# Kernel optimization log

Hardware: AMD Instinct MI355X
Metric: run time of the kernel (lower is better)

## Reference

```python
import jax, jax.numpy as jnp
import numpy as np

N, NFEAT, NHID, NCLASS, NHEAD = 8192, 512, 64, 16, 4
ALPHA = 0.1  # leaky relu slope
NEG = -9e15


def setup_inputs() -> dict:
    key = jax.random.key(0)
    ks = jax.random.split(key, 7)
    x = jax.random.normal(ks[0], (N, NFEAT), dtype=jnp.float32)
    adj = (jax.random.uniform(ks[1], (N, N)) < 0.05).astype(jnp.float32)
    # per-head params: W [H, nfeat, nhid], a [H, 2*nhid] (xavier-ish scale)
    W = jax.random.normal(ks[2], (NHEAD, NFEAT, NHID), dtype=jnp.float32) * (1.0 / np.sqrt(NFEAT))
    a = jax.random.normal(ks[3], (NHEAD, 2 * NHID), dtype=jnp.float32) * (1.0 / np.sqrt(NHID))
    W_out = jax.random.normal(ks[4], (NHEAD * NHID, NCLASS), dtype=jnp.float32) * (1.0 / np.sqrt(NHEAD * NHID))
    a_out = jax.random.normal(ks[5], (2 * NCLASS,), dtype=jnp.float32) * (1.0 / np.sqrt(NCLASS))
    return {"x": x, "adj": adj, "W": W, "a": a, "W_out": W_out, "a_out": a_out}


def _gat_layer(h, adj, Wk, ak):
    """Dense pyGAT GraphAttentionLayer (eval mode, dropout = identity)."""
    d = Wk.shape[1]
    Wh = h @ Wk                         # [N, d]
    f1 = Wh @ ak[:d]                    # [N]
    f2 = Wh @ ak[d:]                    # [N]
    e = jax.nn.leaky_relu(f1[:, None] + f2[None, :], negative_slope=ALPHA)  # [N, N]
    att = jax.nn.softmax(jnp.where(adj > 0, e, NEG), axis=1)
    return att @ Wh                     # [N, d]


def reference(x, adj, W, a, W_out, a_out):
    # eval mode: F.dropout is identity
    heads = jax.vmap(lambda Wk, ak: jax.nn.elu(_gat_layer(x, adj, Wk, ak)))(W, a)  # [H, N, nhid]
    h = jnp.transpose(heads, (1, 0, 2)).reshape(x.shape[0], -1)                    # [N, H*nhid]
    out = jax.nn.elu(_gat_layer(h, adj, W_out, a_out))                             # [N, nclass]
    return jax.nn.log_softmax(out, axis=1)
```

## Files before the change

kernel.cpp:

```cpp
#include <hip/hip_runtime.h>
#include <hip/hip_bf16.h>

#define NN 8192
#define NFEAT 512
#define NHID 64
#define NCLASS 16
#define NHEAD 4
#define ALPHA 0.1f
#define CAP 768

typedef short bf16x8 __attribute__((ext_vector_type(8)));
typedef float f32x4 __attribute__((ext_vector_type(4)));

__device__ __forceinline__ float lrelu(float x) { return fmaxf(x, ALPHA * x); }
__device__ __forceinline__ float elu(float x) { return x > 0.f ? x : __expf(x) - 1.f; }
__device__ __forceinline__ short f2b(float x) {
  union { __bf16 b; short s; } c; c.b = (__bf16)x; return c.s;
}
__device__ __forceinline__ float b2f(short x) {
  union { unsigned int u; float f; } c; c.u = ((unsigned int)(unsigned short)x) << 16; return c.f;
}

#define UPF(w, v, A0, A1)                                  \
  {                                                        \
    const float lo_ = __uint_as_float((v) << 16);          \
    const float hi_ = __uint_as_float((v) & 0xffff0000u);  \
    (A0) += (w) * lo_;                                     \
    (A1) += (w) * hi_;                                     \
  }

__global__ __launch_bounds__(256) void k_wprep(const float* __restrict__ W,
                                               short* __restrict__ WB) {
  __shared__ float t[64][65];
  const int h = blockIdx.y;
  const int k0 = blockIdx.x * 64;
  const int tid = threadIdx.x;
#pragma unroll
  for (int it = 0; it < 16; ++it) {
    const int r = it * 4 + (tid >> 6), c = tid & 63;
    t[r][c] = W[((size_t)h * NFEAT + k0 + r) * NHID + c];
  }
  __syncthreads();
#pragma unroll
  for (int it = 0; it < 16; ++it) {
    const int d = it * 4 + (tid >> 6), k = tid & 63;
    WB[((size_t)h * NHID + d) * NFEAT + k0 + k] = f2b(t[k][d]);
  }
}

__global__ __launch_bounds__(256) void k_mega1(const float* __restrict__ adj,
                                               unsigned int* __restrict__ bmask,
                                               const float* __restrict__ x,
                                               const short* __restrict__ WB,
                                               const float* __restrict__ a,
                                               short* __restrict__ WhB,
                                               float* __restrict__ f1,
                                               float* __restrict__ f2i) {
  const int tid = threadIdx.x;
  if (blockIdx.x < 2048) {
    const float4* a4 = reinterpret_cast<const float4*>(adj);
    const int t0 = blockIdx.x * 256 + tid;
#pragma unroll 4
    for (int it = 0; it < 32; ++it) {
      const int g = it * 524288 + t0;
      const float4 v = a4[g];
      unsigned int nv = (unsigned int)((v.x > 0.f) | ((v.y > 0.f) << 1) |
                                       ((v.z > 0.f) << 2) | ((v.w > 0.f) << 3))
                        << ((tid & 7) * 4);
      nv |= __shfl_xor(nv, 1);
      nv |= __shfl_xor(nv, 2);
      nv |= __shfl_xor(nv, 4);
      if ((tid & 7) == 0) bmask[g >> 3] = nv;
    }
    return;
  }
  __shared__ short tile[64][72];
  const int bid = blockIdx.x - 2048;
  const int h = bid >> 7;
  const int bm = (bid & 127) * 64;
  const int wv = tid >> 6, lane = tid & 63;
  const int mr = lane & 15, kg = lane >> 4;
  f32x4 acc0 = {0.f, 0.f, 0.f, 0.f}, acc1 = acc0, acc2 = acc0, acc3 = acc0;
  const float* ap = x + (size_t)(bm + wv * 16 + mr) * NFEAT + kg * 8;
  const short* bp = WB + ((size_t)h * NHID + mr) * NFEAT + kg * 8;
#pragma unroll 2
  for (int k0 = 0; k0 < NFEAT; k0 += 32) {
    const float4 xa = *reinterpret_cast<const float4*>(ap);
    const float4 xb = *reinterpret_cast<const float4*>(ap + 4);
    bf16x8 af;
    af[0] = f2b(xa.x); af[1] = f2b(xa.y); af[2] = f2b(xa.z); af[3] = f2b(xa.w);
    af[4] = f2b(xb.x); af[5] = f2b(xb.y); af[6] = f2b(xb.z); af[7] = f2b(xb.w);
    const bf16x8 b0 = *reinterpret_cast<const bf16x8*>(bp);
    const bf16x8 b1 = *reinterpret_cast<const bf16x8*>(bp + 16 * NFEAT);
    const bf16x8 b2 = *reinterpret_cast<const bf16x8*>(bp + 32 * NFEAT);
    const bf16x8 b3 = *reinterpret_cast<const bf16x8*>(bp + 48 * NFEAT);
    acc0 = __builtin_amdgcn_mfma_f32_16x16x32_bf16(af, b0, acc0, 0, 0, 0);
    acc1 = __builtin_amdgcn_mfma_f32_16x16x32_bf16(af, b1, acc1, 0, 0, 0);
    acc2 = __builtin_amdgcn_mfma_f32_16x16x32_bf16(af, b2, acc2, 0, 0, 0);
    acc3 = __builtin_amdgcn_mfma_f32_16x16x32_bf16(af, b3, acc3, 0, 0, 0);
    ap += 32; bp += 32;
  }
  float a1v[4], a2v[4];
#pragma unroll
  for (int c = 0; c < 4; ++c) {
    a1v[c] = a[h * 128 + mr + c * 16];
    a2v[c] = a[h * 128 + 64 + mr + c * 16];
  }
#pragma unroll
  for (int q = 0; q < 4; ++q) {
    float s1 = acc0[q] * a1v[0] + acc1[q] * a1v[1] + acc2[q] * a1v[2] + acc3[q] * a1v[3];
    float s2 = acc0[q] * a2v[0] + acc1[q] * a2v[1] + acc2[q] * a2v[2] + acc3[q] * a2v[3];
#pragma unroll
    for (int off = 1; off < 16; off <<= 1) {
      s1 += __shfl_xor(s1, off);
      s2 += __shfl_xor(s2, off);
    }
    if (mr == 0) {
      const int i = bm + wv * 16 + kg * 4 + q;
      f1[h * NN + i] = s1;
      f2i[(size_t)i * 4 + h] = s2;
    }
  }
#pragma unroll
  for (int q = 0; q < 4; ++q) {
    const int r = wv * 16 + kg * 4 + q;
    tile[r][mr +  0] = f2b(acc0[q]);
    tile[r][mr + 16] = f2b(acc1[q]);
    tile[r][mr + 32] = f2b(acc2[q]);
    tile[r][mr + 48] = f2b(acc3[q]);
  }
  __syncthreads();
  {
    const int row = tid >> 2, seg = tid & 3;
    bf16x8 o0, o1;
#pragma unroll
    for (int u = 0; u < 8; ++u) {
      o0[u] = tile[row][seg * 16 + u];
      o1[u] = tile[row][seg * 16 + 8 + u];
    }
    short* dst = WhB + (size_t)(bm + row) * 256 + h * 64 + seg * 16;
    *reinterpret_cast<bf16x8*>(dst) = o0;
    *reinterpret_cast<bf16x8*>(dst + 8) = o1;
  }
}

__global__ __launch_bounds__(256) void k_rmax(const float* __restrict__ src,
                                              float* __restrict__ dst, int n, int stride,
                                              int boff) {
  const float* p = src + (size_t)blockIdx.x * boff;
  float m = -1e30f;
  for (int k = threadIdx.x; k < n; k += 256) m = fmaxf(m, p[(size_t)k * stride]);
#pragma unroll
  for (int off = 32; off; off >>= 1) m = fmaxf(m, __shfl_xor(m, off));
  __shared__ float sm[4];
  if ((threadIdx.x & 63) == 0) sm[threadIdx.x >> 6] = m;
  __syncthreads();
  if (threadIdx.x == 0) dst[blockIdx.x] = fmaxf(fmaxf(sm[0], sm[1]), fmaxf(sm[2], sm[3]));
}

__global__ __launch_bounds__(256) void k_attn1b(const unsigned int* __restrict__ bmask,
                                                const short* __restrict__ WhB,
                                                const float* __restrict__ f1,
                                                const float* __restrict__ f2i,
                                                const float* __restrict__ f2max,
                                                short* __restrict__ hcat) {
  __shared__ unsigned short idx[CAP];
  __shared__ unsigned int widx[NHEAD][CAP];
  __shared__ float swp[4][NHEAD];
  __shared__ float sinv[NHEAD];
  __shared__ int cnt;
  const int i = blockIdx.x;
  const int tid = threadIdx.x;
  const int wv = tid >> 6, lane = tid & 63;
  if (tid == 0) cnt = 0;
  __syncthreads();

  {
    unsigned int word = bmask[(size_t)i * 256 + tid];
    const int c = __popc(word);
    if (c) {
      int base = atomicAdd(&cnt, c);
      const int j0 = tid * 32;
      while (word) {
        const int b = __ffs(word) - 1;
        word &= word - 1;
        if (base < CAP) idx[base++] = (unsigned short)(j0 + b);
      }
    }
  }
  __syncthreads();
  const int n = min(cnt, CAP);

  float f1r[NHEAD], mrow[NHEAD], sw[NHEAD] = {0.f, 0.f, 0.f, 0.f};
#pragma unroll
  for (int h = 0; h < NHEAD; ++h) {
    f1r[h] = f1[h * NN + i];
    mrow[h] = lrelu(f1r[h] + f2max[h]);
  }
  for (int k = tid; k < n; k += 256) {
    const int j = idx[k];
    const float4 f = *reinterpret_cast<const float4*>(f2i + (size_t)j * 4);
    const float w0 = __expf(lrelu(f1r[0] + f.x) - mrow[0]);
    const float w1 = __expf(lrelu(f1r[1] + f.y) - mrow[1]);
    const float w2 = __expf(lrelu(f1r[2] + f.z) - mrow[2]);
    const float w3 = __expf(lrelu(f1r[3] + f.w) - mrow[3]);
    widx[0][k] = ((unsigned int)(unsigned short)f2b(w0) << 16) | (unsigned int)j;
    widx[1][k] = ((unsigned int)(unsigned short)f2b(w1) << 16) | (unsigned int)j;
    widx[2][k] = ((unsigned int)(unsigned short)f2b(w2) << 16) | (unsigned int)j;
    widx[3][k] = ((unsigned int)(unsigned short)f2b(w3) << 16) | (unsigned int)j;
    sw[0] += w0; sw[1] += w1; sw[2] += w2; sw[3] += w3;
  }
#pragma unroll
  for (int off = 32; off; off >>= 1)
#pragma unroll
    for (int h = 0; h < NHEAD; ++h) sw[h] += __shfl_xor(sw[h], off);
  if (lane == 0) {
#pragma unroll
    for (int h = 0; h < NHEAD; ++h) swp[wv][h] = sw[h];
  }
  __syncthreads();
  if (tid < NHEAD) sinv[tid] = 1.f / (swp[0][tid] + swp[1][tid] + swp[2][tid] + swp[3][tid]);

  const int g = lane >> 3, l = lane & 7;
  float acc[8] = {};
  const short* wb = WhB + wv * 64 + l * 8;
  const unsigned int* wrow = widx[wv];
#pragma unroll 2
  for (int k = g; k < n; k += 16) {
    const unsigned int v0 = wrow[k];
    const int k1 = k + 8;
    const unsigned int v1 = (k1 < n) ? wrow[k1] : 0u;
    const int j0 = v0 & 0xffffu;
    const float w0 = __uint_as_float(v0 & 0xffff0000u);
    const int j1 = v1 & 0xffffu;
    const float w1 = __uint_as_float(v1 & 0xffff0000u);
    const uint4 e0 = *reinterpret_cast<const uint4*>(wb + (size_t)j0 * 256);
    const uint4 e1 = *reinterpret_cast<const uint4*>(wb + (size_t)j1 * 256);
    UPF(w0, e0.x, acc[0], acc[1])
    UPF(w0, e0.y, acc[2], acc[3])
    UPF(w0, e0.z, acc[4], acc[5])
    UPF(w0, e0.w, acc[6], acc[7])
    UPF(w1, e1.x, acc[0], acc[1])
    UPF(w1, e1.y, acc[2], acc[3])
    UPF(w1, e1.z, acc[4], acc[5])
    UPF(w1, e1.w, acc[6], acc[7])
  }
  __syncthreads();
#pragma unroll
  for (int u = 0; u < 8; ++u) {
    acc[u] += __shfl_xor(acc[u], 8);
    acc[u] += __shfl_xor(acc[u], 16);
    acc[u] += __shfl_xor(acc[u], 32);
  }
  if (lane < 8) {
    const float iv = sinv[wv];
    bf16x8 o;
#pragma unroll
    for (int u = 0; u < 8; ++u) o[u] = f2b(elu(acc[u] * iv));
    *reinterpret_cast<bf16x8*>(hcat + (size_t)i * 256 + wv * 64 + lane * 8) = o;
  }
}

__global__ __launch_bounds__(256) void k_gemm2(const short* __restrict__ hcat,
                                               const float* __restrict__ Wout,
                                               const float* __restrict__ aout,
                                               short* __restrict__ Wh2B,
                                               float* __restrict__ f1o,
                                               float* __restrict__ f2o) {
  __shared__ float sW[NHEAD * NHID][NCLASS + 1];
  __shared__ float sh[16][NHEAD * NHID + 1];
  const int tid = threadIdx.x;
  const int r = tid >> 4, c = tid & 15;
  const int row = blockIdx.x * 16 + r;
  for (int u = tid; u < 256 * 16; u += 256) sW[u >> 4][u & 15] = Wout[u];
  for (int u = tid; u < 16 * 256; u += 256)
    sh[u >> 8][u & 255] = b2f(hcat[(size_t)(blockIdx.x * 16 + (u >> 8)) * 256 + (u & 255)]);
  __syncthreads();
  float acc = 0.f;
#pragma unroll 8
  for (int f = 0; f < 256; ++f) acc += sh[r][f] * sW[f][c];
  Wh2B[(size_t)row * NCLASS + c] = f2b(acc);
  float s1 = acc * aout[c];
  float s2 = acc * aout[NCLASS + c];
#pragma unroll
  for (int off = 8; off; off >>= 1) { s1 += __shfl_xor(s1, off); s2 += __shfl_xor(s2, off); }
  if (c == 0) { f1o[row] = s1; f2o[row] = s2; }
}

__global__ __launch_bounds__(256) void k_attn2(const unsigned int* __restrict__ bmask,
                                               const short* __restrict__ Wh2B,
                                               const float* __restrict__ f1o,
                                               const float* __restrict__ f2o,
                                               const float* __restrict__ f2omax,
                                               float* __restrict__ out) {
  __shared__ unsigned short idx[CAP];
  __shared__ unsigned int wj[CAP];
  __shared__ float red[4][NCLASS];
  __shared__ float swp[4];
  __shared__ float sinvs;
  __shared__ int cnt;
  const int i = blockIdx.x;
  const int tid = threadIdx.x;
  const int wv = tid >> 6, lane = tid & 63;
  if (tid == 0) cnt = 0;
  __syncthreads();

  {
    unsigned int word = bmask[(size_t)i * 256 + tid];
    const int c = __popc(word);
    if (c) {
      int base = atomicAdd(&cnt, c);
      const int j0 = tid * 32;
      while (word) {
        const int b = __ffs(word) - 1;
        word &= word - 1;
        if (base < CAP) idx[base++] = (unsigned short)(j0 + b);
      }
    }
  }
  __syncthreads();
  const int n = min(cnt, CAP);

  const float f1r = f1o[i];
  const float mrow = lrelu(f1r + f2omax[0]);
  float sw = 0.f;
  for (int k = tid; k < n; k += 256) {
    const int j = idx[k];
    const float w = __expf(lrelu(f1r + f2o[j]) - mrow);
    wj[k] = ((unsigned int)(unsigned short)f2b(w) << 16) | (unsigned int)j;
    sw += w;
  }
#pragma unroll
  for (int off = 32; off; off >>= 1) sw += __shfl_xor(sw, off);
  if (lane == 0) swp[wv] = sw;
  __syncthreads();
  if (tid == 0) sinvs = 1.f / (swp[0] + swp[1] + swp[2] + swp[3]);

  const int g = tid >> 2, gl = tid & 3;
  float acc[4] = {};
  for (int k = g; k < n; k += 128) {
    const unsigned int v0 = wj[k];
    const int k1 = k + 64;
    const unsigned int v1 = (k1 < n) ? wj[k1] : 0u;
    const int j0 = v0 & 0xffffu;
    const float w0 = __uint_as_float(v0 & 0xffff0000u);
    const int j1 = v1 & 0xffffu;
    const float w1 = __uint_as_float(v1 & 0xffff0000u);
    const uint2 e0 = *reinterpret_cast<const uint2*>(Wh2B + (size_t)j0 * NCLASS + gl * 4);
    const uint2 e1 = *reinterpret_cast<const uint2*>(Wh2B + (size_t)j1 * NCLASS + gl * 4);
    UPF(w0, e0.x, acc[0], acc[1])
    UPF(w0, e0.y, acc[2], acc[3])
    UPF(w1, e1.x, acc[0], acc[1])
    UPF(w1, e1.y, acc[2], acc[3])
  }
  __syncthreads();
#pragma unroll
  for (int u = 0; u < 4; ++u) {
    acc[u] += __shfl_xor(acc[u], 4);
    acc[u] += __shfl_xor(acc[u], 8);
    acc[u] += __shfl_xor(acc[u], 16);
    acc[u] += __shfl_xor(acc[u], 32);
  }
  if (lane < 4) {
#pragma unroll
    for (int u = 0; u < 4; ++u) red[wv][lane * 4 + u] = acc[u];
  }
  __syncthreads();
  if (tid < NCLASS) {
    const float s = red[0][tid] + red[1][tid] + red[2][tid] + red[3][tid];
    const float v = elu(s * sinvs);
    float vm = v;
#pragma unroll
    for (int off = 8; off; off >>= 1) vm = fmaxf(vm, __shfl_xor(vm, off, 16));
    float ex = __expf(v - vm);
#pragma unroll
    for (int off = 8; off; off >>= 1) ex += __shfl_xor(ex, off, 16);
    out[(size_t)i * NCLASS + tid] = v - vm - __logf(ex);
  }
}

extern "C" void kernel_launch(void* const* d_in, const int* in_sizes, int n_in,
                              void* d_out, int out_size, void* d_ws, size_t ws_size,
                              hipStream_t stream) {
  const float* x    = (const float*)d_in[0];
  const float* adj  = (const float*)d_in[1];
  const float* W    = (const float*)d_in[2];
  const float* a    = (const float*)d_in[3];
  const float* Wout = (const float*)d_in[4];
  const float* aout = (const float*)d_in[5];
  float* out = (float*)d_out;
  char* ws = (char*)d_ws;
  const size_t MB = 1048576;

  unsigned int* bmask  = (unsigned int*)(ws);
  short* WhB           = (short*)(ws + 8 * MB);
  short* hcat          = (short*)(ws + 12 * MB);
  short* WB            = (short*)(ws + 16 * MB);
  float* f1            = (float*)(ws + 16 * MB + 262144);
  float* f2i           = (float*)(ws + 16 * MB + 393216);
  float* f1o           = (float*)(ws + 16 * MB + 524288);
  float* f2o           = (float*)(ws + 16 * MB + 557056);
  short* Wh2B          = (short*)(ws + 16 * MB + 589824);
  float* f2max         = (float*)(ws + 16 * MB + 851968);
  float* f2omax        = (float*)(ws + 16 * MB + 852032);

  k_wprep<<<dim3(8, 4), 256, 0, stream>>>(W, WB);
  k_mega1<<<2048 + 512, 256, 0, stream>>>(adj, bmask, x, WB, a, WhB, f1, f2i);
  k_rmax<<<NHEAD, 256, 0, stream>>>(f2i, f2max, NN, 4, 1);
  k_attn1b<<<NN, 256, 0, stream>>>(bmask, WhB, f1, f2i, f2max, hcat);
  k_gemm2<<<NN / 16, 256, 0, stream>>>(hcat, Wout, aout, Wh2B, f1o, f2o);
  k_rmax<<<1, 256, 0, stream>>>(f2o, f2omax, NN, 1, 0);
  k_attn2<<<NN, 256, 0, stream>>>(bmask, Wh2B, f1o, f2o, f2omax, out);
}
```

Before: 244.6 us.

## Fuse adjacency bitmask build into layer-1 attention, computing weights during scan

The dense adjacency scan moves out of the first prep kernel and into the per-row layer-1 attention kernel. Each block reads its own adj row with nontemporal loads, writes the bitmask for layer 2, and computes the softmax weights inline while compacting neighbours, so the separate idx pass is gone. The gather loop now reads four packed weight/index entries per uint4 and issues four row loads per iteration. f1 is stored interleaved per node, and one sync is dropped by computing the inverse sum per lane. The adj streaming now sits inside the attention kernel rather than running alongside the GEMM blocks, so it depends on that kernel keeping enough memory traffic in flight.

```diff
diff --git a/kernel.cpp b/kernel.cpp
--- a/kernel.cpp
+++ b/kernel.cpp
@@ -11,6 +11,7 @@
 
 typedef short bf16x8 __attribute__((ext_vector_type(8)));
 typedef float f32x4 __attribute__((ext_vector_type(4)));
+typedef float fv4 __attribute__((ext_vector_type(4)));
 
 __device__ __forceinline__ float lrelu(float x) { return fmaxf(x, ALPHA * x); }
 __device__ __forceinline__ float elu(float x) { return x > 0.f ? x : __expf(x) - 1.f; }
@@ -48,36 +49,17 @@
   }
 }
 
-__global__ __launch_bounds__(256) void k_mega1(const float* __restrict__ adj,
-                                               unsigned int* __restrict__ bmask,
-                                               const float* __restrict__ x,
+__global__ __launch_bounds__(256) void k_prep1(const float* __restrict__ x,
                                                const short* __restrict__ WB,
                                                const float* __restrict__ a,
                                                short* __restrict__ WhB,
-                                               float* __restrict__ f1,
+                                               float* __restrict__ f1i,
                                                float* __restrict__ f2i) {
-  const int tid = threadIdx.x;
-  if (blockIdx.x < 2048) {
-    const float4* a4 = reinterpret_cast<const float4*>(adj);
-    const int t0 = blockIdx.x * 256 + tid;
-#pragma unroll 4
-    for (int it = 0; it < 32; ++it) {
-      const int g = it * 524288 + t0;
-      const float4 v = a4[g];
-      unsigned int nv = (unsigned int)((v.x > 0.f) | ((v.y > 0.f) << 1) |
-                                       ((v.z > 0.f) << 2) | ((v.w > 0.f) << 3))
-                        << ((tid & 7) * 4);
-      nv |= __shfl_xor(nv, 1);
-      nv |= __shfl_xor(nv, 2);
-      nv |= __shfl_xor(nv, 4);
-      if ((tid & 7) == 0) bmask[g >> 3] = nv;
-    }
-    return;
-  }
   __shared__ short tile[64][72];
-  const int bid = blockIdx.x - 2048;
+  const int bid = blockIdx.x;
   const int h = bid >> 7;
   const int bm = (bid & 127) * 64;
+  const int tid = threadIdx.x;
   const int wv = tid >> 6, lane = tid & 63;
   const int mr = lane & 15, kg = lane >> 4;
   f32x4 acc0 = {0.f, 0.f, 0.f, 0.f}, acc1 = acc0, acc2 = acc0, acc3 = acc0;
@@ -117,7 +99,7 @@
     }
     if (mr == 0) {
       const int i = bm + wv * 16 + kg * 4 + q;
-      f1[h * NN + i] = s1;
+      f1i[(size_t)i * 4 + h] = s1;
       f2i[(size_t)i * 4 + h] = s2;
     }
   }
@@ -158,16 +140,15 @@
   if (threadIdx.x == 0) dst[blockIdx.x] = fmaxf(fmaxf(sm[0], sm[1]), fmaxf(sm[2], sm[3]));
 }
 
-__global__ __launch_bounds__(256) void k_attn1b(const unsigned int* __restrict__ bmask,
+__global__ __launch_bounds__(256) void k_attn1f(const float* __restrict__ adj,
                                                 const short* __restrict__ WhB,
-                                                const float* __restrict__ f1,
+                                                const float* __restrict__ f1i,
                                                 const float* __restrict__ f2i,
                                                 const float* __restrict__ f2max,
-                                                short* __restrict__ hcat) {
-  __shared__ unsigned short idx[CAP];
-  __shared__ unsigned int widx[NHEAD][CAP];
-  __shared__ float swp[4][NHEAD];
-  __shared__ float sinv[NHEAD];
+                                                short* __restrict__ hcat,
+                                                unsigned int* __restrict__ bmask) {
+  __shared__ unsigned int widx[NHEAD][CAP + 4];
+  __shared__ float swred[4][NHEAD];
   __shared__ int cnt;
   const int i = blockIdx.x;
   const int tid = threadIdx.x;
@@ -175,77 +156,91 @@
   if (tid == 0) cnt = 0;
   __syncthreads();
 
-  {
-    unsigned int word = bmask[(size_t)i * 256 + tid];
-    const int c = __popc(word);
+  const float4 f1v = *reinterpret_cast<const float4*>(f1i + (size_t)i * 4);
+  const float4 fmx = *reinterpret_cast<const float4*>(f2max);
+  float f1r[4], mrow[4], sw[4] = {0.f, 0.f, 0.f, 0.f};
+  f1r[0] = f1v.x; f1r[1] = f1v.y; f1r[2] = f1v.z; f1r[3] = f1v.w;
+  mrow[0] = lrelu(f1r[0] + fmx.x);
+  mrow[1] = lrelu(f1r[1] + fmx.y);
+  mrow[2] = lrelu(f1r[2] + fmx.z);
+  mrow[3] = lrelu(f1r[3] + fmx.w);
+
+  const fv4* arow = reinterpret_cast<const fv4*>(adj + (size_t)i * NN);
+  const float4* f2i4 = reinterpret_cast<const float4*>(f2i);
+  unsigned int* brow = bmask + (size_t)i * 256;
+#pragma unroll
+  for (int s = 0; s < 8; ++s) {
+    const fv4 v = __builtin_nontemporal_load(arow + s * 256 + tid);
+    const int b0 = v.x > 0.f, b1 = v.y > 0.f, b2 = v.z > 0.f, b3 = v.w > 0.f;
+    unsigned int nv = (unsigned int)(b0 | (b1 << 1) | (b2 << 2) | (b3 << 3)) << ((tid & 7) * 4);
+    nv |= __shfl_xor(nv, 1);
+    nv |= __shfl_xor(nv, 2);
+    nv |= __shfl_xor(nv, 4);
+    if ((tid & 7) == 0) brow[s * 32 + (tid >> 3)] = nv;
+    const int c = b0 + b1 + b2 + b3;
     if (c) {
       int base = atomicAdd(&cnt, c);
-      const int j0 = tid * 32;
-      while (word) {
-        const int b = __ffs(word) - 1;
-        word &= word - 1;
-        if (base < CAP) idx[base++] = (unsigned short)(j0 + b);
+      const int j = s * 1024 + tid * 4;
+      const int bits[4] = {b0, b1, b2, b3};
+#pragma unroll
+      for (int u = 0; u < 4; ++u) {
+        if (bits[u] && base < CAP) {
+          const int jj = j + u;
+          const float4 f = f2i4[jj];
+          const float w0 = __expf(lrelu(f1r[0] + f.x) - mrow[0]);
+          const float w1 = __expf(lrelu(f1r[1] + f.y) - mrow[1]);
+          const float w2 = __expf(lrelu(f1r[2] + f.z) - mrow[2]);
+          const float w3 = __expf(lrelu(f1r[3] + f.w) - mrow[3]);
+          widx[0][base] = ((unsigned int)(unsigned short)f2b(w0) << 16) | (unsigned int)jj;
+          widx[1][base] = ((unsigned int)(unsigned short)f2b(w1) << 16) | (unsigned int)jj;
+          widx[2][base] = ((unsigned int)(unsigned short)f2b(w2) << 16) | (unsigned int)jj;
+          widx[3][base] = ((unsigned int)(unsigned short)f2b(w3) << 16) | (unsigned int)jj;
+          sw[0] += w0; sw[1] += w1; sw[2] += w2; sw[3] += w3;
+          ++base;
+        }
       }
     }
   }
   __syncthreads();
   const int n = min(cnt, CAP);
-
-  float f1r[NHEAD], mrow[NHEAD], sw[NHEAD] = {0.f, 0.f, 0.f, 0.f};
-#pragma unroll
-  for (int h = 0; h < NHEAD; ++h) {
-    f1r[h] = f1[h * NN + i];
-    mrow[h] = lrelu(f1r[h] + f2max[h]);
-  }
-  for (int k = tid; k < n; k += 256) {
-    const int j = idx[k];
-    const float4 f = *reinterpret_cast<const float4*>(f2i + (size_t)j * 4);
-    const float w0 = __expf(lrelu(f1r[0] + f.x) - mrow[0]);
-    const float w1 = __expf(lrelu(f1r[1] + f.y) - mrow[1]);
-    const float w2 = __expf(lrelu(f1r[2] + f.z) - mrow[2]);
-    const float w3 = __expf(lrelu(f1r[3] + f.w) - mrow[3]);
-    widx[0][k] = ((unsigned int)(unsigned short)f2b(w0) << 16) | (unsigned int)j;
-    widx[1][k] = ((unsigned int)(unsigned short)f2b(w1) << 16) | (unsigned int)j;
-    widx[2][k] = ((unsigned int)(unsigned short)f2b(w2) << 16) | (unsigned int)j;
-    widx[3][k] = ((unsigned int)(unsigned short)f2b(w3) << 16) | (unsigned int)j;
-    sw[0] += w0; sw[1] += w1; sw[2] += w2; sw[3] += w3;
-  }
+  if (tid < 16) widx[tid >> 2][n + (tid & 3)] = 0;
 #pragma unroll
   for (int off = 32; off; off >>= 1)
 #pragma unroll
     for (int h = 0; h < NHEAD; ++h) sw[h] += __shfl_xor(sw[h], off);
   if (lane == 0) {
 #pragma unroll
-    for (int h = 0; h < NHEAD; ++h) swp[wv][h] = sw[h];
-  }
-  __syncthreads();
-  if (tid < NHEAD) sinv[tid] = 1.f / (swp[0][tid] + swp[1][tid] + swp[2][tid] + swp[3][tid]);
+    for (int h = 0; h < NHEAD; ++h) swred[wv][h] = sw[h];
+  }
+  __syncthreads();
 
   const int g = lane >> 3, l = lane & 7;
   float acc[8] = {};
   const short* wb = WhB + wv * 64 + l * 8;
   const unsigned int* wrow = widx[wv];
-#pragma unroll 2
-  for (int k = g; k < n; k += 16) {
-    const unsigned int v0 = wrow[k];
-    const int k1 = k + 8;
-    const unsigned int v1 = (k1 < n) ? wrow[k1] : 0u;
-    const int j0 = v0 & 0xffffu;
-    const float w0 = __uint_as_float(v0 & 0xffff0000u);
-    const int j1 = v1 & 0xffffu;
-    const float w1 = __uint_as_float(v1 & 0xffff0000u);
+  for (int k0 = g * 4; k0 < n; k0 += 32) {
+    const uint4 pw = *reinterpret_cast<const uint4*>(wrow + k0);
+    const int j0 = pw.x & 0xffffu;
+    const int j1 = pw.y & 0xffffu;
+    const int j2 = pw.z & 0xffffu;
+    const int j3 = pw.w & 0xffffu;
+    const float w0 = __uint_as_float(pw.x & 0xffff0000u);
+    const float w1 = __uint_as_float(pw.y & 0xffff0000u);
+    const float w2 = __uint_as_float(pw.z & 0xffff0000u);
+    const float w3 = __uint_as_float(pw.w & 0xffff0000u);
     const uint4 e0 = *reinterpret_cast<const uint4*>(wb + (size_t)j0 * 256);
     const uint4 e1 = *reinterpret_cast<const uint4*>(wb + (size_t)j1 * 256);
-    UPF(w0, e0.x, acc[0], acc[1])
-    UPF(w0, e0.y, acc[2], acc[3])
-    UPF(w0, e0.z, acc[4], acc[5])
-    UPF(w0, e0.w, acc[6], acc[7])
-    UPF(w1, e1.x, acc[0], acc[1])
-    UPF(w1, e1.y, acc[2], acc[3])
-    UPF(w1, e1.z, acc[4], acc[5])
-    UPF(w1, e1.w, acc[6], acc[7])
-  }
-  __syncthreads();
+    const uint4 e2 = *reinterpret_cast<const uint4*>(wb + (size_t)j2 * 256);
+    const uint4 e3 = *reinterpret_cast<const uint4*>(wb + (size_t)j3 * 256);
+    UPF(w0, e0.x, acc[0], acc[1]) UPF(w0, e0.y, acc[2], acc[3])
+    UPF(w0, e0.z, acc[4], acc[5]) UPF(w0, e0.w, acc[6], acc[7])
+    UPF(w1, e1.x, acc[0], acc[1]) UPF(w1, e1.y, acc[2], acc[3])
+    UPF(w1, e1.z, acc[4], acc[5]) UPF(w1, e1.w, acc[6], acc[7])
+    UPF(w2, e2.x, acc[0], acc[1]) UPF(w2, e2.y, acc[2], acc[3])
+    UPF(w2, e2.z, acc[4], acc[5]) UPF(w2, e2.w, acc[6], acc[7])
+    UPF(w3, e3.x, acc[0], acc[1]) UPF(w3, e3.y, acc[2], acc[3])
+    UPF(w3, e3.z, acc[4], acc[5]) UPF(w3, e3.w, acc[6], acc[7])
+  }
 #pragma unroll
   for (int u = 0; u < 8; ++u) {
     acc[u] += __shfl_xor(acc[u], 8);
@@ -253,7 +248,7 @@
     acc[u] += __shfl_xor(acc[u], 32);
   }
   if (lane < 8) {
-    const float iv = sinv[wv];
+    const float iv = 1.f / (swred[0][wv] + swred[1][wv] + swred[2][wv] + swred[3][wv]);
     bf16x8 o;
 #pragma unroll
     for (int u = 0; u < 8; ++u) o[u] = f2b(elu(acc[u] * iv));
@@ -396,7 +391,7 @@
   short* WhB           = (short*)(ws + 8 * MB);
   short* hcat          = (short*)(ws + 12 * MB);
   short* WB            = (short*)(ws + 16 * MB);
-  float* f1            = (float*)(ws + 16 * MB + 262144);
+  float* f1i           = (float*)(ws + 16 * MB + 262144);
   float* f2i           = (float*)(ws + 16 * MB + 393216);
   float* f1o           = (float*)(ws + 16 * MB + 524288);
   float* f2o           = (float*)(ws + 16 * MB + 557056);
@@ -405,9 +400,9 @@
   float* f2omax        = (float*)(ws + 16 * MB + 852032);
 
   k_wprep<<<dim3(8, 4), 256, 0, stream>>>(W, WB);
-  k_mega1<<<2048 + 512, 256, 0, stream>>>(adj, bmask, x, WB, a, WhB, f1, f2i);
+  k_prep1<<<512, 256, 0, stream>>>(x, WB, a, WhB, f1i, f2i);
   k_rmax<<<NHEAD, 256, 0, stream>>>(f2i, f2max, NN, 4, 1);
-  k_attn1b<<<NN, 256, 0, stream>>>(bmask, WhB, f1, f2i, f2max, hcat);
+  k_attn1f<<<NN, 256, 0, stream>>>(adj, WhB, f1i, f2i, f2max, hcat, bmask);
   k_gemm2<<<NN / 16, 256, 0, stream>>>(hcat, Wout, aout, Wh2B, f1o, f2o);
   k_rmax<<<1, 256, 0, stream>>>(f2o, f2omax, NN, 1, 0);
   k_attn2<<<NN, 256, 0, stream>>>(bmask, Wh2B, f1o, f2o, f2omax, out);
```

Result: slower. 279.0 us (+14.1%).
